# Kernel optimization log

Measured on AMD Instinct MI355X. Metric: run time of the kernel, lower is better.

Reference implementation:

```python
import jax, jax.numpy as jnp
import numpy as np

N = 200000
E = 3200000
IN_C = 256
HID = 16
OUT_C = 16
EPS = 1e-5


def gcn_conv(x, W, b, src, dst):
    # PyG GCNConv: linear first, then normalized scatter-add with self-loops
    h = x @ W  # [N, F_out]
    loop = jnp.arange(N)
    src2 = jnp.concatenate([src, loop])
    dst2 = jnp.concatenate([dst, loop])
    deg = jax.ops.segment_sum(jnp.ones_like(dst2, dtype=h.dtype), dst2, num_segments=N)
    dinv = jnp.where(deg > 0, jax.lax.rsqrt(deg), 0.0)
    norm = dinv[src2] * dinv[dst2]  # [E+N]
    msg = h[src2] * norm[:, None]
    out = jax.ops.segment_sum(msg, dst2, num_segments=N)
    return out + b


def batch_norm(x, gamma, beta):
    mu = jnp.mean(x, axis=0)
    var = jnp.var(x, axis=0)
    return gamma * (x - mu) * jax.lax.rsqrt(var + EPS) + beta


def setup_inputs() -> dict:
    key = jax.random.key(0)
    ks = jax.random.split(key, 8)
    x = jax.random.normal(ks[0], (N, IN_C), dtype=jnp.float32)
    edge_index = jax.random.randint(ks[1], (2, E), 0, N, dtype=jnp.int64)
    W1 = jax.random.normal(ks[2], (IN_C, HID), dtype=jnp.float32) / np.sqrt(IN_C)
    b1 = jnp.zeros((HID,), jnp.float32)
    g1 = jnp.ones((HID,), jnp.float32)
    be1 = jnp.zeros((HID,), jnp.float32)
    W2 = jax.random.normal(ks[3], (HID, HID), dtype=jnp.float32) / np.sqrt(HID)
    b2 = jnp.zeros((HID,), jnp.float32)
    g2 = jnp.ones((HID,), jnp.float32)
    be2 = jnp.zeros((HID,), jnp.float32)
    W3 = jax.random.normal(ks[4], (HID, OUT_C), dtype=jnp.float32) / np.sqrt(HID)
    b3 = jnp.zeros((OUT_C,), jnp.float32)
    return {"x": x, "edge_index": edge_index, "W1": W1, "b1": b1, "g1": g1,
            "be1": be1, "W2": W2, "b2": b2, "g2": g2, "be2": be2,
            "W3": W3, "b3": b3}


def reference(x, edge_index, W1, b1, g1, be1, W2, b2, g2, be2, W3, b3):
    src, dst = edge_index[0], edge_index[1]
    h = jax.nn.relu(batch_norm(gcn_conv(x, W1, b1, src, dst), g1, be1))
    h = jax.nn.relu(batch_norm(gcn_conv(h, W2, b2, src, dst), g2, be2))
    return gcn_conv(h, W3, b3, src, dst)
```

## Files before the change

### kernel.cpp

```cpp
#include <hip/hip_runtime.h>
#include <hip/hip_bf16.h>
#include <stdint.h>

#define EPSV 1e-5f
#define BKLG 10
#define BK 1024
#define P1CHUNK 16384


__global__ void k_zero(int* __restrict__ indeg, int N, float* __restrict__ stats) {
  int i = blockIdx.x * 256 + threadIdx.x;
  if (i < N) indeg[i] = 0;
  if (i < 64) stats[i] = 0.f;
}


__global__ void k_edges(const int* __restrict__ e32, int E, int N,
                        int* __restrict__ indeg) {
  int i = blockIdx.x * 256 + threadIdx.x;
  if (i >= E) return;
  int d = e32[(size_t)E + i];
  atomicAdd(&indeg[d], 1);
}

__global__ void k_scan1(const int* __restrict__ indeg, int N, int* __restrict__ bsum) {
  __shared__ int sd[256];
  int base = blockIdx.x * 1024;
  int t = threadIdx.x;
  int s = 0;
#pragma unroll
  for (int i = 0; i < 4; i++) {
    int idx = base + t * 4 + i;
    if (idx < N) s += indeg[idx];
  }
  sd[t] = s;
  __syncthreads();
  for (int st = 128; st > 0; st >>= 1) {
    if (t < st) sd[t] += sd[t + st];
    __syncthreads();
  }
  if (t == 0) bsum[blockIdx.x] = sd[0];
}

__global__ void k_scan2(const int* __restrict__ bsum, int B, int* __restrict__ boff) {
  __shared__ int sd[256];
  int t = threadIdx.x;
  int v = (t < B) ? bsum[t] : 0;
  sd[t] = v;
  __syncthreads();
  for (int st = 1; st < 256; st <<= 1) {
    int add = (t >= st) ? sd[t - st] : 0;
    __syncthreads();
    sd[t] += add;
    __syncthreads();
  }
  if (t < B) boff[t] = sd[t] - v;
}

__global__ void k_scan3(const int* __restrict__ indeg, int N, const int* __restrict__ boff,
                        int* __restrict__ offs) {
  __shared__ int sd[256];
  int base = blockIdx.x * 1024;
  int t = threadIdx.x;
  int v[4];
  int s = 0;
#pragma unroll
  for (int i = 0; i < 4; i++) {
    int idx = base + t * 4 + i;
    v[i] = (idx < N) ? indeg[idx] : 0;
    s += v[i];
  }
  sd[t] = s;
  __syncthreads();
  for (int st = 1; st < 256; st <<= 1) {
    int add = (t >= st) ? sd[t - st] : 0;
    __syncthreads();
    sd[t] += add;
    __syncthreads();
  }
  int ex = boff[blockIdx.x] + sd[t] - s;
#pragma unroll
  for (int i = 0; i < 4; i++) {
    int idx = base + t * 4 + i;
    if (idx < N) offs[idx] = ex;
    ex += v[i];
  }
}

__global__ void k_dinv(const int* __restrict__ indeg, int N, int E,
                       float* __restrict__ dinv, int* __restrict__ offs) {
  int i = blockIdx.x * 256 + threadIdx.x;
  if (i == 0) offs[N] = E;
  if (i < N) dinv[i] = rsqrtf((float)(indeg[i] + 1));
}

__global__ void k_ticket(const int* __restrict__ offs, int NB, int* __restrict__ ticket) {
  int b = blockIdx.x * 256 + threadIdx.x;
  if (b < NB) ticket[b] = offs[b << BKLG];
}

__global__ __launch_bounds__(256) void k_bin(const int* __restrict__ e32, int E, int NB,
                                             int* __restrict__ ticket,
                                             unsigned* __restrict__ staged) {
  __shared__ int cnt[256];
  __shared__ int base[256];
  int t = threadIdx.x;
  int e0 = blockIdx.x * P1CHUNK;
  int e1 = min(e0 + P1CHUNK, E);
  if (t < NB) cnt[t] = 0;
  __syncthreads();
  for (int i = e0 + t; i < e1; i += 256) {
    int d = e32[(size_t)E + i];
    atomicAdd(&cnt[d >> BKLG], 1);
  }
  __syncthreads();
  if (t < NB) {
    int c = cnt[t];
    base[t] = c ? atomicAdd(&ticket[t], c) : 0;
    cnt[t] = 0;
  }
  __syncthreads();
  for (int i = e0 + t; i < e1; i += 256) {
    int s = e32[i];
    int d = e32[(size_t)E + i];
    int b = d >> BKLG;
    int l = atomicAdd(&cnt[b], 1);
    staged[base[b] + l] = (unsigned)s | ((unsigned)(d & (BK - 1)) << 18);
  }
}

__global__ __launch_bounds__(256) void k_place(const unsigned* __restrict__ staged,
                                               const int* __restrict__ offs, int N,
                                               int* __restrict__ csr) {
  __shared__ int cur[BK];
  int b = blockIdx.x;
  int n0 = b << BKLG;
  int n1 = min(n0 + BK, N);
  int t = threadIdx.x;
  for (int i = t; i < BK; i += 256) cur[i] = 0;
  __syncthreads();
  int beg = offs[n0], endp = offs[n1];
  for (int j = beg + t; j < endp; j += 256) {
    unsigned v = staged[j];
    int s = (int)(v & 0x3FFFFu);
    int dl = (int)(v >> 18);
    int p = offs[n0 + dl] + atomicAdd(&cur[dl], 1);
    csr[p] = s;
  }
}


__global__ __launch_bounds__(256) void k_gemm1(const float* __restrict__ x,
                                               const float* __restrict__ W,
                                               const float* __restrict__ dinv, int N,
                                               float* __restrict__ hs) {
  int row = blockIdx.x * 256 + threadIdx.x;
  if (row >= N) return;
  const float4* xr = (const float4*)(x + (size_t)row * 256);
  float acc[16];
#pragma unroll
  for (int c = 0; c < 16; c++) acc[c] = 0.f;
#pragma unroll 8
  for (int j = 0; j < 64; j++) {
    float4 v = xr[j];
    const float* w0 = W + j * 64;
#pragma unroll
    for (int c = 0; c < 16; c++) {
      float t0 = fmaf(v.x, w0[c], acc[c]);
      float t1 = fmaf(v.y, w0[16 + c], t0);
      float t2 = fmaf(v.z, w0[32 + c], t1);
      acc[c] = fmaf(v.w, w0[48 + c], t2);
    }
  }
  float dv = dinv[row];
  float4* o4 = (float4*)(hs + (size_t)row * 16);
#pragma unroll
  for (int i = 0; i < 4; i++)
    o4[i] = make_float4(acc[i * 4] * dv, acc[i * 4 + 1] * dv, acc[i * 4 + 2] * dv,
                        acc[i * 4 + 3] * dv);
}

__global__ void k_agg(const float* __restrict__ hs, const int* __restrict__ csr,
                      const int* __restrict__ offs, const float* __restrict__ dinv,
                      const float* __restrict__ bias, int N, float* __restrict__ out) {
  int g = blockIdx.x * 256 + threadIdx.x;
  int node = g >> 2, q = g & 3;
  if (node >= N) return;
  int beg = offs[node], end = offs[node + 1];
  const float4* hs4 = (const float4*)hs;
  float4 a = hs4[(size_t)node * 4 + q];
  for (int j = beg; j < end; j++) {
    int s = csr[j];
    float4 v = hs4[(size_t)s * 4 + q];
    a.x += v.x; a.y += v.y; a.z += v.z; a.w += v.w;
  }
  float dv = dinv[node];
  float4 b = ((const float4*)bias)[q];
  ((float4*)out)[(size_t)node * 4 + q] =
      make_float4(fmaf(a.x, dv, b.x), fmaf(a.y, dv, b.y), fmaf(a.z, dv, b.z), fmaf(a.w, dv, b.w));
}

__global__ void k_bnstats(const float* __restrict__ o, int N, float* __restrict__ stats) {
  __shared__ float ss[256];
  __shared__ float sq[256];
  int t = threadIdx.x;
  int c = t & 15;
  int r = blockIdx.x * 16 + (t >> 4);
  int stride = gridDim.x * 16;
  float s = 0.f, q = 0.f;
  for (; r < N; r += stride) {
    float v = o[(size_t)r * 16 + c];
    s += v;
    q = fmaf(v, v, q);
  }
  ss[t] = s;
  sq[t] = q;
  __syncthreads();
  for (int st = 128; st >= 16; st >>= 1) {
    if (t < st) { ss[t] += ss[t + st]; sq[t] += sq[t + st]; }
    __syncthreads();
  }
  if (t < 16) {
    atomicAdd(&stats[t], ss[t]);
    atomicAdd(&stats[16 + t], sq[t]);
  }
}

__global__ void k_affine(const float* __restrict__ stats, const float* __restrict__ g,
                         const float* __restrict__ be, float invN, float* __restrict__ a,
                         float* __restrict__ s) {
  int c = threadIdx.x;
  if (c < 16) {
    float mean = stats[c] * invN;
    float var = stats[16 + c] * invN - mean * mean;
    float av = g[c] * rsqrtf(var + EPSV);
    a[c] = av;
    s[c] = be[c] - mean * av;
  }
}

__global__ void k_gemm_small(const float* __restrict__ in, const float* __restrict__ a,
                             const float* __restrict__ s, const float* __restrict__ W,
                             const float* __restrict__ dinv, int N, float* __restrict__ out) {
  int row = blockIdx.x * 256 + threadIdx.x;
  if (row >= N) return;
  const float4* in4 = (const float4*)(in + (size_t)row * 16);
  float v[16];
#pragma unroll
  for (int i = 0; i < 4; i++) {
    float4 tv = in4[i];
    v[i * 4 + 0] = tv.x; v[i * 4 + 1] = tv.y; v[i * 4 + 2] = tv.z; v[i * 4 + 3] = tv.w;
  }
#pragma unroll
  for (int c = 0; c < 16; c++) v[c] = fmaxf(fmaf(a[c], v[c], s[c]), 0.f);
  float acc[16];
#pragma unroll
  for (int c = 0; c < 16; c++) acc[c] = 0.f;
#pragma unroll
  for (int k = 0; k < 16; k++) {
#pragma unroll
    for (int c = 0; c < 16; c++) acc[c] = fmaf(v[k], W[k * 16 + c], acc[c]);
  }
  float dv = dinv[row];
  float4* o4 = (float4*)(out + (size_t)row * 16);
#pragma unroll
  for (int i = 0; i < 4; i++)
    o4[i] = make_float4(acc[i * 4] * dv, acc[i * 4 + 1] * dv, acc[i * 4 + 2] * dv,
                        acc[i * 4 + 3] * dv);
}


extern "C" void kernel_launch(void* const* d_in, const int* in_sizes, int n_in,
                              void* d_out, int out_size, void* d_ws, size_t ws_size,
                              hipStream_t stream) {
  const float* x = (const float*)d_in[0];
  const int* eidx = (const int*)d_in[1];
  const float* W1 = (const float*)d_in[2];
  const float* b1 = (const float*)d_in[3];
  const float* g1 = (const float*)d_in[4];
  const float* be1 = (const float*)d_in[5];
  const float* W2 = (const float*)d_in[6];
  const float* b2 = (const float*)d_in[7];
  const float* g2 = (const float*)d_in[8];
  const float* be2 = (const float*)d_in[9];
  const float* W3 = (const float*)d_in[10];
  const float* b3 = (const float*)d_in[11];
  float* out = (float*)d_out;

  int N = in_sizes[0] / 256;
  int E = in_sizes[1] / 2;
  int NB = (N + BK - 1) / BK;

  char* w = (char*)d_ws;
  float* hs = (float*)w;
  int* csr = (int*)(w + (size_t)N * 16 * 4);
  char* p = w + (size_t)N * 16 * 4 + (size_t)E * 4;
  int* offs = (int*)p;
  p += (size_t)(N + 4) * 4;
  float* dinv = (float*)p;
  p += (size_t)N * 4;
  int* indeg = (int*)p;
  p += (size_t)N * 4;
  float* stats1 = (float*)p;
  float* stats2 = stats1 + 32;
  float* a1 = stats2 + 32;
  float* s1 = a1 + 16;
  float* a2 = s1 + 16;
  float* s2 = a2 + 16;
  int* bsum = (int*)(s2 + 16);
  int* boff = bsum + 256;
  int* ticket = boff + 256;

  unsigned* staged = (unsigned*)hs;

  int gE = (E + 255) / 256;
  int gN = (N + 255) / 256;
  int B1 = (N + 1023) / 1024;
  int gQ = (N * 4 + 255) / 256;
  int gB = (E + P1CHUNK - 1) / P1CHUNK;

  k_zero<<<gN, 256, 0, stream>>>(indeg, N, stats1);
  k_edges<<<gE, 256, 0, stream>>>(eidx, E, N, indeg);
  k_scan1<<<B1, 256, 0, stream>>>(indeg, N, bsum);
  k_scan2<<<1, 256, 0, stream>>>(bsum, B1, boff);
  k_scan3<<<B1, 256, 0, stream>>>(indeg, N, boff, offs);
  k_dinv<<<gN, 256, 0, stream>>>(indeg, N, E, dinv, offs);
  k_ticket<<<1, 256, 0, stream>>>(offs, NB, ticket);
  k_bin<<<gB, 256, 0, stream>>>(eidx, E, NB, ticket, staged);
  k_place<<<NB, 256, 0, stream>>>(staged, offs, N, csr);

  float* o = out;
  float invN = 1.f / (float)N;

  k_gemm1<<<gN, 256, 0, stream>>>(x, W1, dinv, N, hs);
  k_agg<<<gQ, 256, 0, stream>>>(hs, csr, offs, dinv, b1, N, o);
  k_bnstats<<<256, 256, 0, stream>>>(o, N, stats1);
  k_affine<<<1, 64, 0, stream>>>(stats1, g1, be1, invN, a1, s1);
  k_gemm_small<<<gN, 256, 0, stream>>>(o, a1, s1, W2, dinv, N, hs);
  k_agg<<<gQ, 256, 0, stream>>>(hs, csr, offs, dinv, b2, N, o);
  k_bnstats<<<256, 256, 0, stream>>>(o, N, stats2);
  k_affine<<<1, 64, 0, stream>>>(stats2, g2, be2, invN, a2, s2);
  k_gemm_small<<<gN, 256, 0, stream>>>(o, a2, s2, W3, dinv, N, hs);
  k_agg<<<gQ, 256, 0, stream>>>(hs, csr, offs, dinv, b3, N, out);
}
```

Measured before the change: 788.5 us.

## Replace global per-node degree histogram with bucket counts and in-block local scan

The CSR build no longer runs a global atomic in-degree count over all edges followed by a three-stage scan. It counts edges per 1024-node bucket using shared-memory atomics and scans those bucket totals in a single block. Each placement block then builds its per-node histogram and exclusive scan locally, and writes the offsets and degree normalisation itself. This removes the scattered global atomics and several small kernel launches, at the cost of an extra pass over the staged edges inside the placement kernel.

```diff
diff --git a/kernel.cpp b/kernel.cpp
--- a/kernel.cpp
+++ b/kernel.cpp
@@ -8,44 +8,38 @@
 #define P1CHUNK 16384
 
 
-__global__ void k_zero(int* __restrict__ indeg, int N, float* __restrict__ stats) {
-  int i = blockIdx.x * 256 + threadIdx.x;
-  if (i < N) indeg[i] = 0;
-  if (i < 64) stats[i] = 0.f;
-}
-
-
-__global__ void k_edges(const int* __restrict__ e32, int E, int N,
-                        int* __restrict__ indeg) {
-  int i = blockIdx.x * 256 + threadIdx.x;
-  if (i >= E) return;
-  int d = e32[(size_t)E + i];
-  atomicAdd(&indeg[d], 1);
-}
-
-__global__ void k_scan1(const int* __restrict__ indeg, int N, int* __restrict__ bsum) {
+__global__ void k_zero(int* __restrict__ bcnt, float* __restrict__ stats) {
+  int t = threadIdx.x;
+  bcnt[t] = 0;
+  if (t < 64) stats[t] = 0.f;
+}
+
+
+__global__ __launch_bounds__(256) void k_bcount(const int* __restrict__ e32, int E, int NB,
+                                                int* __restrict__ bcnt) {
+  __shared__ int cnt[256];
+  int t = threadIdx.x;
+  cnt[t] = 0;
+  __syncthreads();
+  int e0 = blockIdx.x * P1CHUNK;
+  int e1 = min(e0 + P1CHUNK, E);
+  for (int i = e0 + t; i < e1; i += 256) {
+    int d = e32[(size_t)E + i];
+    atomicAdd(&cnt[d >> BKLG], 1);
+  }
+  __syncthreads();
+  if (t < NB) {
+    int c = cnt[t];
+    if (c) atomicAdd(&bcnt[t], c);
+  }
+}
+
+__global__ void k_bscan(const int* __restrict__ bcnt, int NB, int E, int N,
+                        int* __restrict__ ticket, int* __restrict__ bbeg,
+                        int* __restrict__ offs) {
   __shared__ int sd[256];
-  int base = blockIdx.x * 1024;
-  int t = threadIdx.x;
-  int s = 0;
-#pragma unroll
-  for (int i = 0; i < 4; i++) {
-    int idx = base + t * 4 + i;
-    if (idx < N) s += indeg[idx];
-  }
-  sd[t] = s;
-  __syncthreads();
-  for (int st = 128; st > 0; st >>= 1) {
-    if (t < st) sd[t] += sd[t + st];
-    __syncthreads();
-  }
-  if (t == 0) bsum[blockIdx.x] = sd[0];
-}
-
-__global__ void k_scan2(const int* __restrict__ bsum, int B, int* __restrict__ boff) {
-  __shared__ int sd[256];
-  int t = threadIdx.x;
-  int v = (t < B) ? bsum[t] : 0;
+  int t = threadIdx.x;
+  int v = (t < NB) ? bcnt[t] : 0;
   sd[t] = v;
   __syncthreads();
   for (int st = 1; st < 256; st <<= 1) {
@@ -54,49 +48,15 @@
     sd[t] += add;
     __syncthreads();
   }
-  if (t < B) boff[t] = sd[t] - v;
-}
-
-__global__ void k_scan3(const int* __restrict__ indeg, int N, const int* __restrict__ boff,
-                        int* __restrict__ offs) {
-  __shared__ int sd[256];
-  int base = blockIdx.x * 1024;
-  int t = threadIdx.x;
-  int v[4];
-  int s = 0;
-#pragma unroll
-  for (int i = 0; i < 4; i++) {
-    int idx = base + t * 4 + i;
-    v[i] = (idx < N) ? indeg[idx] : 0;
-    s += v[i];
-  }
-  sd[t] = s;
-  __syncthreads();
-  for (int st = 1; st < 256; st <<= 1) {
-    int add = (t >= st) ? sd[t - st] : 0;
-    __syncthreads();
-    sd[t] += add;
-    __syncthreads();
-  }
-  int ex = boff[blockIdx.x] + sd[t] - s;
-#pragma unroll
-  for (int i = 0; i < 4; i++) {
-    int idx = base + t * 4 + i;
-    if (idx < N) offs[idx] = ex;
-    ex += v[i];
-  }
-}
-
-__global__ void k_dinv(const int* __restrict__ indeg, int N, int E,
-                       float* __restrict__ dinv, int* __restrict__ offs) {
-  int i = blockIdx.x * 256 + threadIdx.x;
-  if (i == 0) offs[N] = E;
-  if (i < N) dinv[i] = rsqrtf((float)(indeg[i] + 1));
-}
-
-__global__ void k_ticket(const int* __restrict__ offs, int NB, int* __restrict__ ticket) {
-  int b = blockIdx.x * 256 + threadIdx.x;
-  if (b < NB) ticket[b] = offs[b << BKLG];
+  int ex = sd[t] - v;
+  if (t < NB) {
+    ticket[t] = ex;
+    bbeg[t] = ex;
+  }
+  if (t == 0) {
+    bbeg[NB] = E;
+    offs[N] = E;
+  }
 }
 
 __global__ __launch_bounds__(256) void k_bin(const int* __restrict__ e32, int E, int NB,
@@ -130,22 +90,64 @@
 }
 
 __global__ __launch_bounds__(256) void k_place(const unsigned* __restrict__ staged,
-                                               const int* __restrict__ offs, int N,
-                                               int* __restrict__ csr) {
-  __shared__ int cur[BK];
+                                               const int* __restrict__ bbeg, int N,
+                                               int* __restrict__ csr,
+                                               int* __restrict__ offs,
+                                               float* __restrict__ dinv) {
+  __shared__ int hist[BK];
+  __shared__ int lpos[BK];
+  __shared__ int sd[256];
   int b = blockIdx.x;
   int n0 = b << BKLG;
-  int n1 = min(n0 + BK, N);
-  int t = threadIdx.x;
-  for (int i = t; i < BK; i += 256) cur[i] = 0;
-  __syncthreads();
-  int beg = offs[n0], endp = offs[n1];
+  int t = threadIdx.x;
+  for (int i = t; i < BK; i += 256) hist[i] = 0;
+  __syncthreads();
+  int beg = bbeg[b], endp = bbeg[b + 1];
   for (int j = beg + t; j < endp; j += 256) {
     unsigned v = staged[j];
-    int s = (int)(v & 0x3FFFFu);
+    atomicAdd(&hist[v >> 18], 1);
+  }
+  __syncthreads();
+  int i0 = t * 4;
+  int h0 = hist[i0], h1 = hist[i0 + 1], h2 = hist[i0 + 2], h3 = hist[i0 + 3];
+  int s = h0 + h1 + h2 + h3;
+  sd[t] = s;
+  __syncthreads();
+  for (int st = 1; st < 256; st <<= 1) {
+    int add = (t >= st) ? sd[t - st] : 0;
+    __syncthreads();
+    sd[t] += add;
+    __syncthreads();
+  }
+  int ex = sd[t] - s;
+  int l0 = ex, l1 = ex + h0, l2 = l1 + h1, l3 = l2 + h2;
+  lpos[i0] = beg + l0;
+  lpos[i0 + 1] = beg + l1;
+  lpos[i0 + 2] = beg + l2;
+  lpos[i0 + 3] = beg + l3;
+  int node = n0 + i0;
+  if (node < N) {
+    offs[node] = beg + l0;
+    dinv[node] = rsqrtf((float)(h0 + 1));
+  }
+  if (node + 1 < N) {
+    offs[node + 1] = beg + l1;
+    dinv[node + 1] = rsqrtf((float)(h1 + 1));
+  }
+  if (node + 2 < N) {
+    offs[node + 2] = beg + l2;
+    dinv[node + 2] = rsqrtf((float)(h2 + 1));
+  }
+  if (node + 3 < N) {
+    offs[node + 3] = beg + l3;
+    dinv[node + 3] = rsqrtf((float)(h3 + 1));
+  }
+  __syncthreads();
+  for (int j = beg + t; j < endp; j += 256) {
+    unsigned v = staged[j];
     int dl = (int)(v >> 18);
-    int p = offs[n0 + dl] + atomicAdd(&cur[dl], 1);
-    csr[p] = s;
+    int p = atomicAdd(&lpos[dl], 1);
+    csr[p] = (int)(v & 0x3FFFFu);
   }
 }
 
@@ -299,35 +301,27 @@
   p += (size_t)(N + 4) * 4;
   float* dinv = (float*)p;
   p += (size_t)N * 4;
-  int* indeg = (int*)p;
-  p += (size_t)N * 4;
   float* stats1 = (float*)p;
   float* stats2 = stats1 + 32;
   float* a1 = stats2 + 32;
   float* s1 = a1 + 16;
   float* a2 = s1 + 16;
   float* s2 = a2 + 16;
-  int* bsum = (int*)(s2 + 16);
-  int* boff = bsum + 256;
-  int* ticket = boff + 256;
+  int* bcnt = (int*)(s2 + 16);
+  int* bbeg = bcnt + 256;
+  int* ticket = bbeg + 260;
 
   unsigned* staged = (unsigned*)hs;
 
-  int gE = (E + 255) / 256;
   int gN = (N + 255) / 256;
-  int B1 = (N + 1023) / 1024;
   int gQ = (N * 4 + 255) / 256;
   int gB = (E + P1CHUNK - 1) / P1CHUNK;
 
-  k_zero<<<gN, 256, 0, stream>>>(indeg, N, stats1);
-  k_edges<<<gE, 256, 0, stream>>>(eidx, E, N, indeg);
-  k_scan1<<<B1, 256, 0, stream>>>(indeg, N, bsum);
-  k_scan2<<<1, 256, 0, stream>>>(bsum, B1, boff);
-  k_scan3<<<B1, 256, 0, stream>>>(indeg, N, boff, offs);
-  k_dinv<<<gN, 256, 0, stream>>>(indeg, N, E, dinv, offs);
-  k_ticket<<<1, 256, 0, stream>>>(offs, NB, ticket);
+  k_zero<<<1, 256, 0, stream>>>(bcnt, stats1);
+  k_bcount<<<gB, 256, 0, stream>>>(eidx, E, NB, bcnt);
+  k_bscan<<<1, 256, 0, stream>>>(bcnt, NB, E, N, ticket, bbeg, offs);
   k_bin<<<gB, 256, 0, stream>>>(eidx, E, NB, ticket, staged);
-  k_place<<<NB, 256, 0, stream>>>(staged, offs, N, csr);
+  k_place<<<NB, 256, 0, stream>>>(staged, bbeg, N, csr, offs, dinv);
 
   float* o = out;
   float invN = 1.f / (float)N;
```

After: 694.1 us. 1.14x faster.
